# Optimization experiments

Hardware: AMD Instinct MI355X
Metric: run time of the kernel (lower is better)

The kernel has to match this reference:

```python
import jax, jax.numpy as jnp
import numpy as np
from jax import lax

K_ADA = 0.1
EPS = 1e-5
B, G = 2, 96
C0, C1, C2, C3, F = 1, 16, 32, 64, 64


def adanorm(x, g):
    # AdaNorm over the last (channel) axis: w * (1 - k*xn) * xn
    mean = x.mean(-1, keepdims=True)
    var = ((x - mean) ** 2).mean(-1, keepdims=True) + EPS
    xn = (x - mean) * lax.rsqrt(var)
    return g * (1.0 - K_ADA * xn) * xn


def conv3d(x, w, b, stride):
    # x: [B,D,H,W,Cin], w: [3,3,3,Cin,Cout], padding 1
    y = lax.conv_general_dilated(x, w, (stride,) * 3, [(1, 1)] * 3,
                                 dimension_numbers=('NDHWC', 'DHWIO', 'NDHWC'))
    return y + b


def downsample_mask(m):
    # active output sites of SparseConv3d(k=3, s=2, p=1): any active input in window
    return lax.reduce_window(m, 0.0, lax.max, (1, 3, 3, 3), (1, 2, 2, 2),
                             [(0, 0), (1, 1), (1, 1), (1, 1)])


def setup_inputs() -> dict:
    key = jax.random.key(0)
    ks = jax.random.split(key, 20)
    mask = (jax.random.uniform(ks[0], (B, G, G, G)) < 0.05).astype(jnp.float32)
    x = jax.random.normal(ks[1], (B, G, G, G, C0), jnp.float32) * mask[..., None]

    def wconv(k, cin, cout):
        return jax.random.normal(k, (3, 3, 3, cin, cout), jnp.float32) / np.sqrt(27.0 * cin)

    inp = {'x': x, 'mask': mask}
    chans = [(C0, C1), (C1, C2), (C2, C2), (C2, C3), (C3, C3)]
    for i, (ci, co) in enumerate(chans, start=1):
        inp[f'w{i}'] = wconv(ks[2 * i], ci, co)
        inp[f'b{i}'] = jax.random.normal(ks[2 * i + 1], (co,), jnp.float32) * 0.01
        inp[f'g{i}'] = jnp.ones((co,), jnp.float32)
    inp['wh'] = jax.random.normal(ks[12], (C3, F), jnp.float32) / np.sqrt(C3)
    inp['bh'] = jax.random.normal(ks[13], (F,), jnp.float32) * 0.01
    inp['gh'] = jnp.ones((F,), jnp.float32)
    return inp


def reference(x, mask, w1, b1, g1, w2, b2, g2, w3, b3, g3, w4, b4, g4, w5, b5, g5, wh, bh, gh):
    m1 = mask
    h = conv3d(x, w1, b1, 1) * m1[..., None]            # SubMConv3d
    h = jax.nn.relu(adanorm(h, g1)) * m1[..., None]
    m2 = downsample_mask(m1)
    h = conv3d(h, w2, b2, 2) * m2[..., None]            # SparseConv3d s=2
    h = jax.nn.relu(adanorm(h, g2)) * m2[..., None]
    h = conv3d(h, w3, b3, 1) * m2[..., None]            # SubMConv3d
    h = jax.nn.relu(adanorm(h, g3)) * m2[..., None]
    m3 = downsample_mask(m2)
    h = conv3d(h, w4, b4, 2) * m3[..., None]            # SparseConv3d s=2
    h = jax.nn.relu(adanorm(h, g4)) * m3[..., None]
    h = conv3d(h, w5, b5, 1) * m3[..., None]            # SubMConv3d
    h = jax.nn.relu(adanorm(h, g5)) * m3[..., None]
    # SparseGlobalMaxPool over active voxels
    neg = jnp.asarray(-3.0e38, h.dtype)
    pooled = jnp.where(m3[..., None] > 0, h, neg).max(axis=(1, 2, 3))  # [B, C3]
    # head: Linear -> AdaNorm -> ReLU -> Dropout(eval = identity)
    out = jax.nn.relu(adanorm(pooled @ wh + bh, gh))
    return out
```

## Files before the change

### kernel.cpp

```cpp
#include <hip/hip_runtime.h>
#include <math.h>

#define K_ADA 0.1f
#define NEPS 1e-5f

typedef __attribute__((ext_vector_type(8))) short short8;
typedef __attribute__((ext_vector_type(4))) float f32x4;
typedef unsigned short ushort_t;

__device__ __forceinline__ ushort_t f2b(float f) {
    union { float f; unsigned u; } v; v.f = f;
    unsigned r = (v.u + 0x7fffu + ((v.u >> 16) & 1u)) >> 16;
    return (ushort_t)r;
}

__device__ __forceinline__ float wave_sum64(float v) {
#pragma unroll
    for (int m = 1; m < 64; m <<= 1) v += __shfl_xor(v, m, 64);
    return v;
}

template <int CIN, int COUT>
__device__ __forceinline__ void pack_w_el(const float* __restrict__ w,
                                          ushort_t* __restrict__ wp, int t)
{
    constexpr int NKH = CIN / 32;
    constexpr int NCT = COUT / 16;
    int jj = t & 7;
    int lane = (t >> 3) & 63;
    int rest = t >> 9;
    int kh = rest % NKH;
    int rest2 = rest / NKH;
    int ct = rest2 % NCT;
    int tap = rest2 / NCT;
    int cin = kh * 32 + (lane >> 4) * 8 + jj;
    int cout = ct * 16 + (lane & 15);
    wp[t] = f2b(w[(tap * CIN + cin) * COUT + cout]);
}

__global__ __launch_bounds__(256) void prep_k(
    const float* __restrict__ w1, const float* __restrict__ w2,
    const float* __restrict__ w3, const float* __restrict__ w4,
    const float* __restrict__ w5, const float* __restrict__ m1,
    ushort_t* __restrict__ wp1, ushort_t* __restrict__ wp2,
    ushort_t* __restrict__ wp3, ushort_t* __restrict__ wp4,
    ushort_t* __restrict__ wp5, float* __restrict__ m2,
    float* __restrict__ zeropad)
{
    int t = blockIdx.x * 256 + threadIdx.x;
    if (t < 512) {
        int jj = t & 7;
        int lane = t >> 3;
        int tap = (lane >> 4) * 8 + jj;
        int cout = lane & 15;
        wp1[t] = (tap < 27) ? f2b(w1[tap * 16 + cout]) : (ushort_t)0;
    } else if (t < 14848) {
        int u = t - 512;
        int jj = u & 7;
        int lane = (u >> 3) & 63;
        int rest = u >> 9;
        int ct = rest & 1;
        int p = rest >> 1;
        int tap = 2 * p + (lane >> 5);
        int cin = ((lane >> 4) & 1) * 8 + jj;
        int cout = ct * 16 + (lane & 15);
        wp2[u] = (tap < 27) ? f2b(w2[(tap * 16 + cin) * 32 + cout]) : (ushort_t)0;
    } else if (t < 42496) {
        pack_w_el<32, 32>(w3, wp3, t - 14848);
    } else if (t < 97792) {
        pack_w_el<32, 64>(w4, wp4, t - 42496);
    } else if (t < 208384) {
        pack_w_el<64, 64>(w5, wp5, t - 97792);
    } else if (t < 429568) {
        int v = t - 208384;
        constexpr int GO = 48, GI = 96;
        int b = v / (GO * GO * GO);
        int r = v % (GO * GO * GO);
        int d = r / (GO * GO), h = (r / GO) % GO, x = r % GO;
        float mx = 0.f;
        for (int kd = 0; kd < 3; ++kd) {
            int zd = 2 * d + kd - 1; if ((unsigned)zd >= GI) continue;
            for (int kh = 0; kh < 3; ++kh) {
                int zh = 2 * h + kh - 1; if ((unsigned)zh >= GI) continue;
                for (int kw = 0; kw < 3; ++kw) {
                    int zx = 2 * x + kw - 1; if ((unsigned)zx >= GI) continue;
                    mx = fmaxf(mx, m1[((b * GI + zd) * GI + zh) * GI + zx]);
                }
            }
        }
        m2[v] = mx;
    } else if (t < 429576) {
        zeropad[t - 429568] = 0.f;
    }
}

template <int GO, int GI>
__global__ __launch_bounds__(256) void dmask_k(const float* __restrict__ mi,
                                               float* __restrict__ mo)
{
    constexpr int N = 2 * GO * GO * GO;
    int v = blockIdx.x * 256 + threadIdx.x;
    if (v >= N) return;
    int b = v / (GO * GO * GO);
    int r = v % (GO * GO * GO);
    int d = r / (GO * GO), h = (r / GO) % GO, x = r % GO;
    float mx = 0.f;
    for (int kd = 0; kd < 3; ++kd) {
        int zd = 2 * d + kd - 1; if ((unsigned)zd >= GI) continue;
        for (int kh = 0; kh < 3; ++kh) {
            int zh = 2 * h + kh - 1; if ((unsigned)zh >= GI) continue;
            for (int kw = 0; kw < 3; ++kw) {
                int zx = 2 * x + kw - 1; if ((unsigned)zx >= GI) continue;
                mx = fmaxf(mx, mi[((b * GI + zd) * GI + zh) * GI + zx]);
            }
        }
    }
    mo[v] = mx;
}

__global__ __launch_bounds__(256) void conv1_mfma_k(const float* __restrict__ x,
                                                    const float* __restrict__ m1,
                                                    const ushort_t* __restrict__ wp1,
                                                    const float* __restrict__ bias,
                                                    const float* __restrict__ gain,
                                                    const float* __restrict__ zerof,
                                                    ushort_t* __restrict__ h1b)
{
    constexpr int G = 96, G3 = G * G * G;
    int wave = (blockIdx.x * 256 + threadIdx.x) >> 6;
    int lane = threadIdx.x & 63;
    int m = lane & 15, q = lane >> 4;
    int vb = wave * 16;
    int vm = vb + m;
    int b = vm / G3;
    int rr = vm % G3;
    int dm = rr / (G * G), hm = (rr / G) % G, xm = rr % G;

    bool act = (m1[vm] != 0.f);
    if (!__any(act)) {
        reinterpret_cast<unsigned long long*>(h1b + (size_t)vb * 16)[lane] = 0ull;
        return;
    }

    float xs[8];
#pragma unroll
    for (int j = 0; j < 8; ++j) {
        int k = q * 8 + j;
        int kd = k / 9, kh = (k / 3) % 3, kw = k % 3;
        int id = dm + kd - 1, ih = hm + kh - 1, ix = xm + kw - 1;
        bool ok = (k < 27) && ((unsigned)id < (unsigned)G) &&
                  ((unsigned)ih < (unsigned)G) && ((unsigned)ix < (unsigned)G);
        const float* xp = ok ? (x + (((size_t)b * G + id) * G + ih) * G + ix) : zerof;
        xs[j] = *xp;
    }
    ushort_t av[8];
#pragma unroll
    for (int j = 0; j < 8; ++j) av[j] = f2b(xs[j]);
    short8 a = *reinterpret_cast<short8*>(av);
    short8 bfr = *reinterpret_cast<const short8*>(wp1 + lane * 8);
    f32x4 acc = {0.f, 0.f, 0.f, 0.f};
    acc = __builtin_amdgcn_mfma_f32_16x16x32_bf16(a, bfr, acc, 0, 0, 0);

    float bn = bias[m], gn = gain[m];
#pragma unroll
    for (int i = 0; i < 4; ++i) {
        int w = vb + q * 4 + i;
        float xv = acc[i] + bn;
        float s = xv;
#pragma unroll
        for (int mk = 1; mk < 16; mk <<= 1) s += __shfl_xor(s, mk, 64);
        float mean = s * (1.f / 16.f);
        float dd = xv - mean;
        float ss = dd * dd;
#pragma unroll
        for (int mk = 1; mk < 16; mk <<= 1) ss += __shfl_xor(ss, mk, 64);
        float rs = rsqrtf(ss * (1.f / 16.f) + NEPS);
        float xn = dd * rs;
        float o = fmaxf(gn * (1.f - K_ADA * xn) * xn, 0.f);
        h1b[(size_t)w * 16 + m] = (m1[w] != 0.f) ? f2b(o) : (ushort_t)0;
    }
}

__device__ __forceinline__ void norm32_epilogue(
    f32x4 acc0, f32x4 acc1, int vb, int q, int n,
    const float* __restrict__ bias, const float* __restrict__ gain,
    const float* __restrict__ mask, ushort_t* __restrict__ outb)
{
    float b0 = bias[n], b1 = bias[16 + n];
    float g0 = gain[n], g1 = gain[16 + n];
#pragma unroll
    for (int i = 0; i < 4; ++i) {
        int w = vb + q * 4 + i;
        float x0 = acc0[i] + b0;
        float x1 = acc1[i] + b1;
        float s = x0 + x1;
#pragma unroll
        for (int mk = 1; mk < 16; mk <<= 1) s += __shfl_xor(s, mk, 64);
        float mean = s * (1.f / 32.f);
        float d0 = x0 - mean, d1 = x1 - mean;
        float ss = d0 * d0 + d1 * d1;
#pragma unroll
        for (int mk = 1; mk < 16; mk <<= 1) ss += __shfl_xor(ss, mk, 64);
        float rs = rsqrtf(ss * (1.f / 32.f) + NEPS);
        float mv = mask[w];
        float xn0 = d0 * rs, xn1 = d1 * rs;
        float o0 = fmaxf(g0 * (1.f - K_ADA * xn0) * xn0, 0.f);
        float o1 = fmaxf(g1 * (1.f - K_ADA * xn1) * xn1, 0.f);
        if (mv == 0.f) { o0 = 0.f; o1 = 0.f; }
        outb[(size_t)w * 32 + n]      = f2b(o0);
        outb[(size_t)w * 32 + 16 + n] = f2b(o1);
    }
}

__global__ __launch_bounds__(256) void conv2_mfma_k(
    const ushort_t* __restrict__ h1b, const ushort_t* __restrict__ wp2,
    const float* __restrict__ bias, const float* __restrict__ gain,
    const float* __restrict__ m2, const ushort_t* __restrict__ zp,
    ushort_t* __restrict__ h2b)
{
    constexpr int G = 48, GI = 96, G3 = G * G * G;
    int wave = (blockIdx.x * 256 + threadIdx.x) >> 6;
    int lane = threadIdx.x & 63;
    int m = lane & 15, q = lane >> 4;
    int vb = wave * 32;
    int tq = q >> 1;
    int hq = q & 1;

    int vmA = vb + m, vmB = vb + 16 + m;
    int bA = vmA / G3, rA = vmA % G3;
    int dA = rA / (G * G), hA = (rA / G) % G, xA = rA % G;
    int bB = vmB / G3, rB = vmB % G3;
    int dB = rB / (G * G), hB = (rB / G) % G, xB = rB % G;

    f32x4 acc00 = {0.f, 0.f, 0.f, 0.f}, acc01 = acc00, acc10 = acc00, acc11 = acc00;
#pragma unroll
    for (int p = 0; p < 14; ++p) {
        int tap = 2 * p + tq;
        int kd = tap / 9, kh = (tap / 3) % 3, kw = tap % 3;
        int idA = 2 * dA + kd - 1, ihA = 2 * hA + kh - 1, ixA = 2 * xA + kw - 1;
        int idB = 2 * dB + kd - 1, ihB = 2 * hB + kh - 1, ixB = 2 * xB + kw - 1;
        bool okA = (tap < 27) && ((unsigned)idA < (unsigned)GI) &&
                   ((unsigned)ihA < (unsigned)GI) && ((unsigned)ixA < (unsigned)GI);
        bool okB = (tap < 27) && ((unsigned)idB < (unsigned)GI) &&
                   ((unsigned)ihB < (unsigned)GI) && ((unsigned)ixB < (unsigned)GI);
        size_t nvA = (((size_t)bA * GI + idA) * GI + ihA) * GI + ixA;
        size_t nvB = (((size_t)bB * GI + idB) * GI + ihB) * GI + ixB;
        const ushort_t* pA = okA ? (h1b + nvA * 16 + hq * 8) : zp;
        const ushort_t* pB = okB ? (h1b + nvB * 16 + hq * 8) : zp;
        short8 a0 = *reinterpret_cast<const short8*>(pA);
        short8 a1 = *reinterpret_cast<const short8*>(pB);
        short8 bv0 = *reinterpret_cast<const short8*>(wp2 + ((size_t)(p * 2 + 0) * 64 + lane) * 8);
        short8 bv1 = *reinterpret_cast<const short8*>(wp2 + ((size_t)(p * 2 + 1) * 64 + lane) * 8);
        acc00 = __builtin_amdgcn_mfma_f32_16x16x32_bf16(a0, bv0, acc00, 0, 0, 0);
        acc01 = __builtin_amdgcn_mfma_f32_16x16x32_bf16(a0, bv1, acc01, 0, 0, 0);
        acc10 = __builtin_amdgcn_mfma_f32_16x16x32_bf16(a1, bv0, acc10, 0, 0, 0);
        acc11 = __builtin_amdgcn_mfma_f32_16x16x32_bf16(a1, bv1, acc11, 0, 0, 0);
    }
    norm32_epilogue(acc00, acc01, vb,      q, m, bias, gain, m2, h2b);
    norm32_epilogue(acc10, acc11, vb + 16, q, m, bias, gain, m2, h2b);
}

__global__ __launch_bounds__(256, 4) void conv3_mfma_k(
    const ushort_t* __restrict__ h2b, const ushort_t* __restrict__ wp3,
    const float* __restrict__ bias, const float* __restrict__ gain,
    const float* __restrict__ m2, const ushort_t* __restrict__ zp,
    ushort_t* __restrict__ h3b)
{
    constexpr int G = 48, G3 = G * G * G;
    int wave = (blockIdx.x * 256 + threadIdx.x) >> 6;
    int lane = threadIdx.x & 63;
    int m = lane & 15, q = lane >> 4;
    int vb = wave * 32;

    int vmA = vb + m, vmB = vb + 16 + m;
    int bA = vmA / G3, rA = vmA % G3;
    int dA = rA / (G * G), hA = (rA / G) % G, xA = rA % G;
    int bB = vmB / G3, rB = vmB % G3;
    int dB = rB / (G * G), hB = (rB / G) % G, xB = rB % G;

    f32x4 acc00 = {0.f, 0.f, 0.f, 0.f}, acc01 = acc00, acc10 = acc00, acc11 = acc00;
#pragma unroll
    for (int tap = 0; tap < 27; ++tap) {
        const int kd = tap / 9, kh = (tap / 3) % 3, kw = tap % 3;
        int idA = dA + kd - 1, ihA = hA + kh - 1, ixA = xA + kw - 1;
        int idB = dB + kd - 1, ihB = hB + kh - 1, ixB = xB + kw - 1;
        bool okA = ((unsigned)idA < (unsigned)G) && ((unsigned)ihA < (unsigned)G) &&
                   ((unsigned)ixA < (unsigned)G);
        bool okB = ((unsigned)idB < (unsigned)G) && ((unsigned)ihB < (unsigned)G) &&
                   ((unsigned)ixB < (unsigned)G);
        size_t nvA = (((size_t)bA * G + idA) * G + ihA) * G + ixA;
        size_t nvB = (((size_t)bB * G + idB) * G + ihB) * G + ixB;
        const ushort_t* pA = okA ? (h2b + nvA * 32 + q * 8) : zp;
        const ushort_t* pB = okB ? (h2b + nvB * 32 + q * 8) : zp;
        short8 a0 = *reinterpret_cast<const short8*>(pA);
        short8 a1 = *reinterpret_cast<const short8*>(pB);
        short8 bv0 = *reinterpret_cast<const short8*>(wp3 + ((size_t)(tap * 2 + 0) * 64 + lane) * 8);
        short8 bv1 = *reinterpret_cast<const short8*>(wp3 + ((size_t)(tap * 2 + 1) * 64 + lane) * 8);
        acc00 = __builtin_amdgcn_mfma_f32_16x16x32_bf16(a0, bv0, acc00, 0, 0, 0);
        acc01 = __builtin_amdgcn_mfma_f32_16x16x32_bf16(a0, bv1, acc01, 0, 0, 0);
        acc10 = __builtin_amdgcn_mfma_f32_16x16x32_bf16(a1, bv0, acc10, 0, 0, 0);
        acc11 = __builtin_amdgcn_mfma_f32_16x16x32_bf16(a1, bv1, acc11, 0, 0, 0);
    }
    norm32_epilogue(acc00, acc01, vb,      q, m, bias, gain, m2, h3b);
    norm32_epilogue(acc10, acc11, vb + 16, q, m, bias, gain, m2, h3b);
}

template <int G_IN, int CIN, int STRIDE, bool OUTB>
__global__ __launch_bounds__(256, 4) void conv45_tile_k(
    const ushort_t* __restrict__ Ab, const ushort_t* __restrict__ Wp,
    const float* __restrict__ bias, const float* __restrict__ gain,
    const float* __restrict__ mask,
    ushort_t* __restrict__ outb, float* __restrict__ outf)
{
    constexpr int G = 24;
    constexpr int NKH = CIN / 32;
    constexpr int NCH = CIN / 8;
    constexpr int PADC = NCH + 1;
    constexpr int HD = STRIDE + 3;
    constexpr int HH = STRIDE + 3;
    constexpr int HX = 3 * STRIDE + 3;
    constexpr int NHV = HD * HH * HX;
    constexpr int NCHUNK = NHV * NCH;

    __shared__ __align__(16) ushort_t halo[NHV * PADC * 8];
    __shared__ float nbuf[16][65];

    int bid = blockIdx.x;
    int b = bid / 864;
    int r = bid % 864;
    int td = r / 72, th = (r / 6) % 12, tx = r % 6;
    int d0 = 2 * td, h0 = 2 * th, x0 = 4 * tx;
    int bd = d0 * STRIDE - 1, bh = h0 * STRIDE - 1, bx = x0 * STRIDE - 1;

    for (int c = threadIdx.x; c < NCHUNK; c += 256) {
        int hv = c / NCH, j = c % NCH;
        int gd = bd + hv / (HH * HX);
        int gh = bh + (hv / HX) % HH;
        int gx = bx + hv % HX;
        short8 val = {0, 0, 0, 0, 0, 0, 0, 0};
        if ((unsigned)gd < (unsigned)G_IN && (unsigned)gh < (unsigned)G_IN &&
            (unsigned)gx < (unsigned)G_IN)
            val = *reinterpret_cast<const short8*>(
                Ab + ((((size_t)b * G_IN + gd) * G_IN + gh) * G_IN + gx) * CIN + j * 8);
        *reinterpret_cast<short8*>(halo + ((size_t)hv * PADC + j) * 8) = val;
    }
    __syncthreads();

    int ct = threadIdx.x >> 6;
    int lane = threadIdx.x & 63;
    int m = lane & 15, q = lane >> 4;
    int md = (m >> 3) & 1, mh = (m >> 2) & 1, mx = m & 3;

    f32x4 acc = {0.f, 0.f, 0.f, 0.f};
    constexpr int NT = 27 * NKH;
    constexpr int GSZ = 9;
#pragma unroll
    for (int g = 0; g < NT / GSZ; ++g) {
        short8 ab[GSZ], bb[GSZ];
#pragma unroll
        for (int j = 0; j < GSZ; ++j) {
            int it = g * GSZ + j;
            int tap = it / NKH, k2 = it % NKH;
            const int kd = tap / 9, kh = (tap / 3) % 3, kw = tap % 3;
            int hv = ((md * STRIDE + kd) * HH + (mh * STRIDE + kh)) * HX +
                     (mx * STRIDE + kw);
            ab[j] = *reinterpret_cast<const short8*>(
                halo + ((size_t)hv * PADC + k2 * 4 + q) * 8);
            bb[j] = *reinterpret_cast<const short8*>(
                Wp + (((size_t)(tap * 4 + ct) * NKH + k2) * 64 + lane) * 8);
        }
#pragma unroll
        for (int j = 0; j < GSZ; ++j)
            acc = __builtin_amdgcn_mfma_f32_16x16x32_bf16(ab[j], bb[j], acc, 0, 0, 0);
    }

    float bn = bias[ct * 16 + m];
#pragma unroll
    for (int i = 0; i < 4; ++i) nbuf[q * 4 + i][ct * 16 + m] = acc[i] + bn;
    __syncthreads();

    float gn = gain[lane];
#pragma unroll
    for (int i = 0; i < 4; ++i) {
        int vloc = ct * 4 + i;
        int vd = d0 + ((vloc >> 3) & 1);
        int vh = h0 + ((vloc >> 2) & 1);
        int vx = x0 + (vloc & 3);
        int w = ((b * G + vd) * G + vh) * G + vx;
        float val = nbuf[vloc][lane];
        float mean = wave_sum64(val) * (1.f / 64.f);
        float dd = val - mean;
        float var = wave_sum64(dd * dd) * (1.f / 64.f) + NEPS;
        float xn = dd * rsqrtf(var);
        float o = fmaxf(gn * (1.f - K_ADA * xn) * xn, 0.f);
        if (mask[w] == 0.f) o = 0.f;
        if (OUTB) outb[(size_t)w * 64 + lane] = f2b(o);
        else      outf[(size_t)w * 64 + lane] = o;
    }
}

__global__ __launch_bounds__(256) void pool1_k(const float* __restrict__ h5,
                                               float* __restrict__ partials)
{
    int chunk = blockIdx.x % 54;
    int b = blockIdx.x / 54;
    int c = threadIdx.x & 63;
    int s = threadIdx.x >> 6;
    const float* base = h5 + ((size_t)b * 13824 + chunk * 256) * 64;
    float mx = 0.f;
#pragma unroll 4
    for (int v = s; v < 256; v += 4) mx = fmaxf(mx, base[v * 64 + c]);
    __shared__ float red[256];
    red[threadIdx.x] = mx;
    __syncthreads();
    if (s == 0)
        partials[blockIdx.x * 64 + c] =
            fmaxf(fmaxf(red[c], red[64 + c]), fmaxf(red[128 + c], red[192 + c]));
}

__global__ __launch_bounds__(128) void pool2_head_k(const float* __restrict__ partials,
                                                    const float* __restrict__ wh,
                                                    const float* __restrict__ bh,
                                                    const float* __restrict__ gh,
                                                    float* __restrict__ out)
{
    __shared__ float pooled[2][64];
    int t = threadIdx.x;
    int b = t >> 6;
    int f = t & 63;
    float mx = 0.f;
    for (int p = 0; p < 54; ++p) mx = fmaxf(mx, partials[(b * 54 + p) * 64 + f]);
    pooled[b][f] = mx;
    __syncthreads();
    float acc = bh[f];
#pragma unroll
    for (int k = 0; k < 64; ++k) acc += pooled[b][k] * wh[k * 64 + f];
    float mean = wave_sum64(acc) * (1.f / 64.f);
    float dd = acc - mean;
    float var = wave_sum64(dd * dd) * (1.f / 64.f) + NEPS;
    float xn = dd * rsqrtf(var);
    float val = gh[f] * (1.f - K_ADA * xn) * xn;
    out[t] = fmaxf(val, 0.f);
}

extern "C" void kernel_launch(void* const* d_in, const int* in_sizes, int n_in,
                              void* d_out, int out_size, void* d_ws, size_t ws_size,
                              hipStream_t stream)
{
    const float* x  = (const float*)d_in[0];
    const float* m1 = (const float*)d_in[1];
    const float* w1 = (const float*)d_in[2];
    const float* b1 = (const float*)d_in[3];
    const float* g1 = (const float*)d_in[4];
    const float* w2 = (const float*)d_in[5];
    const float* b2 = (const float*)d_in[6];
    const float* g2 = (const float*)d_in[7];
    const float* w3 = (const float*)d_in[8];
    const float* b3 = (const float*)d_in[9];
    const float* g3 = (const float*)d_in[10];
    const float* w4 = (const float*)d_in[11];
    const float* b4 = (const float*)d_in[12];
    const float* g4 = (const float*)d_in[13];
    const float* w5 = (const float*)d_in[14];
    const float* b5 = (const float*)d_in[15];
    const float* g5 = (const float*)d_in[16];
    const float* wh = (const float*)d_in[17];
    const float* bh = (const float*)d_in[18];
    const float* gh = (const float*)d_in[19];
    float* out = (float*)d_out;

    float* ws = (float*)d_ws;
    ushort_t* h1b = (ushort_t*)ws;
    ushort_t* h2b = (ushort_t*)(ws + 14155776);
    ushort_t* h3b = (ushort_t*)(ws + 17694720);
    ushort_t* h4b = (ushort_t*)(ws + 21233664);
    float* h5 = ws + 22118400;
    float* m2 = ws + 23887872;
    float* m3 = ws + 24109056;
    float* partials = ws + 24136704;
    ushort_t* wp1 = (ushort_t*)(ws + 24143616);
    ushort_t* wp2 = (ushort_t*)(ws + 24143872);
    ushort_t* wp3 = (ushort_t*)(ws + 24151040);
    ushort_t* wp4 = (ushort_t*)(ws + 24164864);
    ushort_t* wp5 = (ushort_t*)(ws + 24192512);
    float* zeropad = ws + 24247808;

    prep_k<<<1679, 256, 0, stream>>>(w1, w2, w3, w4, w5, m1,
                                     wp1, wp2, wp3, wp4, wp5, m2, zeropad);
    dmask_k<24, 48><<<108, 256, 0, stream>>>(m2, m3);

    const ushort_t* zp = (const ushort_t*)zeropad;
    conv1_mfma_k<<<27648, 256, 0, stream>>>(x, m1, wp1, b1, g1, zeropad, h1b);
    conv2_mfma_k<<<1728, 256, 0, stream>>>(h1b, wp2, b2, g2, m2, zp, h2b);
    conv3_mfma_k<<<1728, 256, 0, stream>>>(h2b, wp3, b3, g3, m2, zp, h3b);
    conv45_tile_k<48, 32, 2, true><<<1728, 256, 0, stream>>>(h3b, wp4, b4, g4, m3, h4b, nullptr);
    conv45_tile_k<24, 64, 1, false><<<1728, 256, 0, stream>>>(h4b, wp5, b5, g5, m3, nullptr, h5);

    pool1_k<<<108, 256, 0, stream>>>(h5, partials);
    pool2_head_k<<<1, 128, 0, stream>>>(partials, wh, bh, gh, out);
}
```

Before: 270.6 us.

## Compact active voxels for conv1 and stage LDS halo tiles for conv2/conv3

Conv1 is split into two kernels. A fill kernel zeros the output and builds a compacted list of active voxels using ballot and an atomic counter. A grid-stride kernel then runs the MFMA only on 16-voxel chunks of that list, skipping the partially inactive groups the old kernel still computed. Conv2 and conv3 are rewritten to load a 4x4x4 output tile's input halo into shared memory once and read all 27 taps from LDS, instead of issuing redundant global gathers per tap. This adds atomics, an extra launch and LDS pressure, and reuses the h2b workspace region to hold the list.

```diff
diff --git a/kernel.cpp b/kernel.cpp
--- a/kernel.cpp
+++ b/kernel.cpp
@@ -18,6 +18,10 @@
 #pragma unroll
     for (int m = 1; m < 64; m <<= 1) v += __shfl_xor(v, m, 64);
     return v;
+}
+
+__host__ __device__ constexpr int tapd2(int tap) {
+    return tap >= 27 ? 0 : (tap / 9) * 81 + ((tap / 3) % 3) * 9 + (tap % 3);
 }
 
 template <int CIN, int COUT>
@@ -45,7 +49,7 @@
     ushort_t* __restrict__ wp1, ushort_t* __restrict__ wp2,
     ushort_t* __restrict__ wp3, ushort_t* __restrict__ wp4,
     ushort_t* __restrict__ wp5, float* __restrict__ m2,
-    float* __restrict__ zeropad)
+    float* __restrict__ zeropad, int* __restrict__ counter)
 {
     int t = blockIdx.x * 256 + threadIdx.x;
     if (t < 512) {
@@ -91,6 +95,8 @@
         m2[v] = mx;
     } else if (t < 429576) {
         zeropad[t - 429568] = 0.f;
+    } else if (t == 429576) {
+        *counter = 0;
     }
 }
 
@@ -118,191 +124,264 @@
     mo[v] = mx;
 }
 
-__global__ __launch_bounds__(256) void conv1_mfma_k(const float* __restrict__ x,
-                                                    const float* __restrict__ m1,
-                                                    const ushort_t* __restrict__ wp1,
-                                                    const float* __restrict__ bias,
-                                                    const float* __restrict__ gain,
-                                                    const float* __restrict__ zerof,
-                                                    ushort_t* __restrict__ h1b)
+__global__ __launch_bounds__(256) void conv1_fill_k(const float* __restrict__ m1,
+                                                    ushort_t* __restrict__ h1b,
+                                                    int* __restrict__ list,
+                                                    int* __restrict__ counter)
+{
+    int v = blockIdx.x * 256 + threadIdx.x;
+    const short8 z = {0, 0, 0, 0, 0, 0, 0, 0};
+    short8* hp = reinterpret_cast<short8*>(h1b + (size_t)v * 16);
+    hp[0] = z; hp[1] = z;
+    bool act = (m1[v] != 0.f);
+    unsigned long long msk = __ballot(act);
+    int lane = threadIdx.x & 63;
+    int base = 0;
+    int cnt = __popcll(msk);
+    if (lane == 0 && cnt) base = atomicAdd(counter, cnt);
+    base = __shfl(base, 0, 64);
+    if (act) {
+        int pre = __popcll(msk & ((1ull << lane) - 1ull));
+        list[base + pre] = v;
+    }
+}
+
+__global__ __launch_bounds__(256) void conv1_act_k(const float* __restrict__ x,
+                                                   const int* __restrict__ list,
+                                                   const int* __restrict__ counter,
+                                                   const ushort_t* __restrict__ wp1,
+                                                   const float* __restrict__ bias,
+                                                   const float* __restrict__ gain,
+                                                   const float* __restrict__ zerof,
+                                                   ushort_t* __restrict__ h1b)
 {
     constexpr int G = 96, G3 = G * G * G;
-    int wave = (blockIdx.x * 256 + threadIdx.x) >> 6;
+    int nact = counter[0];
+    if (nact <= 0) return;
+    int gwave = (blockIdx.x * 256 + threadIdx.x) >> 6;
+    int nwaves = gridDim.x * 4;
     int lane = threadIdx.x & 63;
     int m = lane & 15, q = lane >> 4;
-    int vb = wave * 16;
-    int vm = vb + m;
-    int b = vm / G3;
-    int rr = vm % G3;
-    int dm = rr / (G * G), hm = (rr / G) % G, xm = rr % G;
-
-    bool act = (m1[vm] != 0.f);
-    if (!__any(act)) {
-        reinterpret_cast<unsigned long long*>(h1b + (size_t)vb * 16)[lane] = 0ull;
-        return;
-    }
-
-    float xs[8];
-#pragma unroll
-    for (int j = 0; j < 8; ++j) {
-        int k = q * 8 + j;
-        int kd = k / 9, kh = (k / 3) % 3, kw = k % 3;
-        int id = dm + kd - 1, ih = hm + kh - 1, ix = xm + kw - 1;
-        bool ok = (k < 27) && ((unsigned)id < (unsigned)G) &&
-                  ((unsigned)ih < (unsigned)G) && ((unsigned)ix < (unsigned)G);
-        const float* xp = ok ? (x + (((size_t)b * G + id) * G + ih) * G + ix) : zerof;
-        xs[j] = *xp;
-    }
-    ushort_t av[8];
-#pragma unroll
-    for (int j = 0; j < 8; ++j) av[j] = f2b(xs[j]);
-    short8 a = *reinterpret_cast<short8*>(av);
+    int nchunk = (nact + 15) >> 4;
+    float bn = bias[m], gn = gain[m];
     short8 bfr = *reinterpret_cast<const short8*>(wp1 + lane * 8);
-    f32x4 acc = {0.f, 0.f, 0.f, 0.f};
-    acc = __builtin_amdgcn_mfma_f32_16x16x32_bf16(a, bfr, acc, 0, 0, 0);
-
-    float bn = bias[m], gn = gain[m];
-#pragma unroll
-    for (int i = 0; i < 4; ++i) {
-        int w = vb + q * 4 + i;
-        float xv = acc[i] + bn;
-        float s = xv;
-#pragma unroll
-        for (int mk = 1; mk < 16; mk <<= 1) s += __shfl_xor(s, mk, 64);
-        float mean = s * (1.f / 16.f);
-        float dd = xv - mean;
-        float ss = dd * dd;
-#pragma unroll
-        for (int mk = 1; mk < 16; mk <<= 1) ss += __shfl_xor(ss, mk, 64);
-        float rs = rsqrtf(ss * (1.f / 16.f) + NEPS);
-        float xn = dd * rs;
-        float o = fmaxf(gn * (1.f - K_ADA * xn) * xn, 0.f);
-        h1b[(size_t)w * 16 + m] = (m1[w] != 0.f) ? f2b(o) : (ushort_t)0;
-    }
-}
-
-__device__ __forceinline__ void norm32_epilogue(
-    f32x4 acc0, f32x4 acc1, int vb, int q, int n,
-    const float* __restrict__ bias, const float* __restrict__ gain,
-    const float* __restrict__ mask, ushort_t* __restrict__ outb)
-{
-    float b0 = bias[n], b1 = bias[16 + n];
-    float g0 = gain[n], g1 = gain[16 + n];
-#pragma unroll
-    for (int i = 0; i < 4; ++i) {
-        int w = vb + q * 4 + i;
-        float x0 = acc0[i] + b0;
-        float x1 = acc1[i] + b1;
-        float s = x0 + x1;
-#pragma unroll
-        for (int mk = 1; mk < 16; mk <<= 1) s += __shfl_xor(s, mk, 64);
-        float mean = s * (1.f / 32.f);
-        float d0 = x0 - mean, d1 = x1 - mean;
-        float ss = d0 * d0 + d1 * d1;
-#pragma unroll
-        for (int mk = 1; mk < 16; mk <<= 1) ss += __shfl_xor(ss, mk, 64);
-        float rs = rsqrtf(ss * (1.f / 32.f) + NEPS);
-        float mv = mask[w];
-        float xn0 = d0 * rs, xn1 = d1 * rs;
-        float o0 = fmaxf(g0 * (1.f - K_ADA * xn0) * xn0, 0.f);
-        float o1 = fmaxf(g1 * (1.f - K_ADA * xn1) * xn1, 0.f);
-        if (mv == 0.f) { o0 = 0.f; o1 = 0.f; }
-        outb[(size_t)w * 32 + n]      = f2b(o0);
-        outb[(size_t)w * 32 + 16 + n] = f2b(o1);
-    }
-}
-
-__global__ __launch_bounds__(256) void conv2_mfma_k(
+
+    for (int chunk = gwave; chunk < nchunk; chunk += nwaves) {
+        int idx = chunk * 16 + m;
+        int vm = list[min(idx, nact - 1)];
+        int b = vm / G3;
+        int rr = vm % G3;
+        int dm = rr / (G * G), hm = (rr / G) % G, xm = rr % G;
+
+        float xs[8];
+#pragma unroll
+        for (int j = 0; j < 8; ++j) {
+            int k = q * 8 + j;
+            int kd = k / 9, kh = (k / 3) % 3, kw = k % 3;
+            int id = dm + kd - 1, ih = hm + kh - 1, ix = xm + kw - 1;
+            bool ok = (k < 27) && ((unsigned)id < (unsigned)G) &&
+                      ((unsigned)ih < (unsigned)G) && ((unsigned)ix < (unsigned)G);
+            const float* xp = ok ? (x + (((size_t)b * G + id) * G + ih) * G + ix) : zerof;
+            xs[j] = *xp;
+        }
+        ushort_t av[8];
+#pragma unroll
+        for (int j = 0; j < 8; ++j) av[j] = f2b(xs[j]);
+        short8 a = *reinterpret_cast<short8*>(av);
+        f32x4 acc = {0.f, 0.f, 0.f, 0.f};
+        acc = __builtin_amdgcn_mfma_f32_16x16x32_bf16(a, bfr, acc, 0, 0, 0);
+
+#pragma unroll
+        for (int i = 0; i < 4; ++i) {
+            int oidx = chunk * 16 + q * 4 + i;
+            float xv = acc[i] + bn;
+            float s = xv;
+#pragma unroll
+            for (int mk = 1; mk < 16; mk <<= 1) s += __shfl_xor(s, mk, 64);
+            float mean = s * (1.f / 16.f);
+            float dd = xv - mean;
+            float ss = dd * dd;
+#pragma unroll
+            for (int mk = 1; mk < 16; mk <<= 1) ss += __shfl_xor(ss, mk, 64);
+            float rs = rsqrtf(ss * (1.f / 16.f) + NEPS);
+            float xn = dd * rs;
+            float o = fmaxf(gn * (1.f - K_ADA * xn) * xn, 0.f);
+            if (oidx < nact) {
+                int w = list[oidx];
+                h1b[(size_t)w * 16 + m] = f2b(o);
+            }
+        }
+    }
+}
+
+__global__ __launch_bounds__(256, 4) void conv2_tile_k(
     const ushort_t* __restrict__ h1b, const ushort_t* __restrict__ wp2,
     const float* __restrict__ bias, const float* __restrict__ gain,
     const float* __restrict__ m2, const ushort_t* __restrict__ zp,
     ushort_t* __restrict__ h2b)
 {
-    constexpr int G = 48, GI = 96, G3 = G * G * G;
-    int wave = (blockIdx.x * 256 + threadIdx.x) >> 6;
+    constexpr int GI = 96, G = 48;
+    __shared__ __align__(16) ushort_t halo[729 * 3 * 8];
+
+    int bid = blockIdx.x;
+    int b = bid / 1728;
+    int r = bid % 1728;
+    int td = r / 144, th = (r / 12) % 12, tx = r % 12;
+    int d0 = 4 * td, h0 = 4 * th, x0 = 4 * tx;
+    int bd = 2 * d0 - 1, bh = 2 * h0 - 1, bx = 2 * x0 - 1;
+
+    for (int c = threadIdx.x; c < 1458; c += 256) {
+        int hv = c >> 1, j = c & 1;
+        int gd = bd + hv / 81;
+        int gh = bh + (hv / 9) % 9;
+        int gx = bx + hv % 9;
+        bool ok = ((unsigned)gd < (unsigned)GI) && ((unsigned)gh < (unsigned)GI) &&
+                  ((unsigned)gx < (unsigned)GI);
+        const ushort_t* p = ok ? (h1b + ((((size_t)b * GI + gd) * GI + gh) * GI + gx) * 16 + j * 8) : zp;
+        *reinterpret_cast<short8*>(halo + ((size_t)hv * 3 + j) * 8) =
+            *reinterpret_cast<const short8*>(p);
+    }
+    __syncthreads();
+
+    int wv = threadIdx.x >> 6;
     int lane = threadIdx.x & 63;
     int m = lane & 15, q = lane >> 4;
-    int vb = wave * 32;
-    int tq = q >> 1;
-    int hq = q & 1;
-
-    int vmA = vb + m, vmB = vb + 16 + m;
-    int bA = vmA / G3, rA = vmA % G3;
-    int dA = rA / (G * G), hA = (rA / G) % G, xA = rA % G;
-    int bB = vmB / G3, rB = vmB % G3;
-    int dB = rB / (G * G), hB = (rB / G) % G, xB = rB % G;
-
-    f32x4 acc00 = {0.f, 0.f, 0.f, 0.f}, acc01 = acc00, acc10 = acc00, acc11 = acc00;
-#pragma unroll
-    for (int p = 0; p < 14; ++p) {
-        int tap = 2 * p + tq;
-        int kd = tap / 9, kh = (tap / 3) % 3, kw = tap % 3;
-        int idA = 2 * dA + kd - 1, ihA = 2 * hA + kh - 1, ixA = 2 * xA + kw - 1;
-        int idB = 2 * dB + kd - 1, ihB = 2 * hB + kh - 1, ixB = 2 * xB + kw - 1;
-        bool okA = (tap < 27) && ((unsigned)idA < (unsigned)GI) &&
-                   ((unsigned)ihA < (unsigned)GI) && ((unsigned)ixA < (unsigned)GI);
-        bool okB = (tap < 27) && ((unsigned)idB < (unsigned)GI) &&
-                   ((unsigned)ihB < (unsigned)GI) && ((unsigned)ixB < (unsigned)GI);
-        size_t nvA = (((size_t)bA * GI + idA) * GI + ihA) * GI + ixA;
-        size_t nvB = (((size_t)bB * GI + idB) * GI + ihB) * GI + ixB;
-        const ushort_t* pA = okA ? (h1b + nvA * 16 + hq * 8) : zp;
-        const ushort_t* pB = okB ? (h1b + nvB * 16 + hq * 8) : zp;
-        short8 a0 = *reinterpret_cast<const short8*>(pA);
-        short8 a1 = *reinterpret_cast<const short8*>(pB);
-        short8 bv0 = *reinterpret_cast<const short8*>(wp2 + ((size_t)(p * 2 + 0) * 64 + lane) * 8);
-        short8 bv1 = *reinterpret_cast<const short8*>(wp2 + ((size_t)(p * 2 + 1) * 64 + lane) * 8);
-        acc00 = __builtin_amdgcn_mfma_f32_16x16x32_bf16(a0, bv0, acc00, 0, 0, 0);
-        acc01 = __builtin_amdgcn_mfma_f32_16x16x32_bf16(a0, bv1, acc01, 0, 0, 0);
-        acc10 = __builtin_amdgcn_mfma_f32_16x16x32_bf16(a1, bv0, acc10, 0, 0, 0);
-        acc11 = __builtin_amdgcn_mfma_f32_16x16x32_bf16(a1, bv1, acc11, 0, 0, 0);
-    }
-    norm32_epilogue(acc00, acc01, vb,      q, m, bias, gain, m2, h2b);
-    norm32_epilogue(acc10, acc11, vb + 16, q, m, bias, gain, m2, h2b);
-}
-
-__global__ __launch_bounds__(256, 4) void conv3_mfma_k(
+    int mh = m >> 2, mx = m & 3;
+    int tq = q >> 1, hq = q & 1;
+    int hbase = 162 * wv + 18 * mh + 2 * mx;
+
+    f32x4 accs[2];
+#pragma unroll
+    for (int ct = 0; ct < 2; ++ct) {
+        f32x4 acc = {0.f, 0.f, 0.f, 0.f};
+#pragma unroll
+        for (int g = 0; g < 2; ++g) {
+            short8 ab[7], bb[7];
+#pragma unroll
+            for (int j = 0; j < 7; ++j) {
+                const int p = g * 7 + j;
+                int hv = hbase + (tq ? tapd2(2 * p + 1) : tapd2(2 * p));
+                ab[j] = *reinterpret_cast<const short8*>(halo + ((size_t)hv * 3 + hq) * 8);
+                bb[j] = *reinterpret_cast<const short8*>(
+                    wp2 + ((size_t)(p * 2 + ct) * 64 + lane) * 8);
+            }
+#pragma unroll
+            for (int j = 0; j < 7; ++j)
+                acc = __builtin_amdgcn_mfma_f32_16x16x32_bf16(ab[j], bb[j], acc, 0, 0, 0);
+        }
+        accs[ct] = acc;
+    }
+
+    float b0 = bias[m], b1 = bias[16 + m];
+    float g0 = gain[m], g1 = gain[16 + m];
+#pragma unroll
+    for (int i = 0; i < 4; ++i) {
+        int rr2 = q * 4 + i;
+        int w = ((b * G + d0 + wv) * G + h0 + (rr2 >> 2)) * G + x0 + (rr2 & 3);
+        float xv0 = accs[0][i] + b0;
+        float xv1 = accs[1][i] + b1;
+        float s = xv0 + xv1;
+#pragma unroll
+        for (int mk = 1; mk < 16; mk <<= 1) s += __shfl_xor(s, mk, 64);
+        float mean = s * (1.f / 32.f);
+        float dd0 = xv0 - mean, dd1 = xv1 - mean;
+        float ss = dd0 * dd0 + dd1 * dd1;
+#pragma unroll
+        for (int mk = 1; mk < 16; mk <<= 1) ss += __shfl_xor(ss, mk, 64);
+        float rs = rsqrtf(ss * (1.f / 32.f) + NEPS);
+        float mv = m2[w];
+        float xn0 = dd0 * rs, xn1 = dd1 * rs;
+        float o0 = fmaxf(g0 * (1.f - K_ADA * xn0) * xn0, 0.f);
+        float o1 = fmaxf(g1 * (1.f - K_ADA * xn1) * xn1, 0.f);
+        if (mv == 0.f) { o0 = 0.f; o1 = 0.f; }
+        h2b[(size_t)w * 32 + m]      = f2b(o0);
+        h2b[(size_t)w * 32 + 16 + m] = f2b(o1);
+    }
+}
+
+__global__ __launch_bounds__(256, 4) void conv3_tile_k(
     const ushort_t* __restrict__ h2b, const ushort_t* __restrict__ wp3,
     const float* __restrict__ bias, const float* __restrict__ gain,
     const float* __restrict__ m2, const ushort_t* __restrict__ zp,
     ushort_t* __restrict__ h3b)
 {
-    constexpr int G = 48, G3 = G * G * G;
-    int wave = (blockIdx.x * 256 + threadIdx.x) >> 6;
+    constexpr int G = 48;
+    __shared__ __align__(16) ushort_t halo[216 * 5 * 8];
+
+    int bid = blockIdx.x;
+    int b = bid / 1728;
+    int r = bid % 1728;
+    int td = r / 144, th = (r / 12) % 12, tx = r % 12;
+    int d0 = 4 * td, h0 = 4 * th, x0 = 4 * tx;
+    int bd = d0 - 1, bh = h0 - 1, bx = x0 - 1;
+
+    for (int c = threadIdx.x; c < 864; c += 256) {
+        int hv = c >> 2, j = c & 3;
+        int gd = bd + hv / 36;
+        int gh = bh + (hv / 6) % 6;
+        int gx = bx + hv % 6;
+        bool ok = ((unsigned)gd < (unsigned)G) && ((unsigned)gh < (unsigned)G) &&
+                  ((unsigned)gx < (unsigned)G);
+        const ushort_t* p = ok ? (h2b + ((((size_t)b * G + gd) * G + gh) * G + gx) * 32 + j * 8) : zp;
+        *reinterpret_cast<short8*>(halo + ((size_t)hv * 5 + j) * 8) =
+            *reinterpret_cast<const short8*>(p);
+    }
+    __syncthreads();
+
+    int wv = threadIdx.x >> 6;
     int lane = threadIdx.x & 63;
     int m = lane & 15, q = lane >> 4;
-    int vb = wave * 32;
-
-    int vmA = vb + m, vmB = vb + 16 + m;
-    int bA = vmA / G3, rA = vmA % G3;
-    int dA = rA / (G * G), hA = (rA / G) % G, xA = rA % G;
-    int bB = vmB / G3, rB = vmB % G3;
-    int dB = rB / (G * G), hB = (rB / G) % G, xB = rB % G;
-
-    f32x4 acc00 = {0.f, 0.f, 0.f, 0.f}, acc01 = acc00, acc10 = acc00, acc11 = acc00;
-#pragma unroll
-    for (int tap = 0; tap < 27; ++tap) {
-        const int kd = tap / 9, kh = (tap / 3) % 3, kw = tap % 3;
-        int idA = dA + kd - 1, ihA = hA + kh - 1, ixA = xA + kw - 1;
-        int idB = dB + kd - 1, ihB = hB + kh - 1, ixB = xB + kw - 1;
-        bool okA = ((unsigned)idA < (unsigned)G) && ((unsigned)ihA < (unsigned)G) &&
-                   ((unsigned)ixA < (unsigned)G);
-        bool okB = ((unsigned)idB < (unsigned)G) && ((unsigned)ihB < (unsigned)G) &&
-                   ((unsigned)ixB < (unsigned)G);
-        size_t nvA = (((size_t)bA * G + idA) * G + ihA) * G + ixA;
-        size_t nvB = (((size_t)bB * G + idB) * G + ihB) * G + ixB;
-        const ushort_t* pA = okA ? (h2b + nvA * 32 + q * 8) : zp;
-        const ushort_t* pB = okB ? (h2b + nvB * 32 + q * 8) : zp;
-        short8 a0 = *reinterpret_cast<const short8*>(pA);
-        short8 a1 = *reinterpret_cast<const short8*>(pB);
-        short8 bv0 = *reinterpret_cast<const short8*>(wp3 + ((size_t)(tap * 2 + 0) * 64 + lane) * 8);
-        short8 bv1 = *reinterpret_cast<const short8*>(wp3 + ((size_t)(tap * 2 + 1) * 64 + lane) * 8);
-        acc00 = __builtin_amdgcn_mfma_f32_16x16x32_bf16(a0, bv0, acc00, 0, 0, 0);
-        acc01 = __builtin_amdgcn_mfma_f32_16x16x32_bf16(a0, bv1, acc01, 0, 0, 0);
-        acc10 = __builtin_amdgcn_mfma_f32_16x16x32_bf16(a1, bv0, acc10, 0, 0, 0);
-        acc11 = __builtin_amdgcn_mfma_f32_16x16x32_bf16(a1, bv1, acc11, 0, 0, 0);
-    }
-    norm32_epilogue(acc00, acc01, vb,      q, m, bias, gain, m2, h3b);
-    norm32_epilogue(acc10, acc11, vb + 16, q, m, bias, gain, m2, h3b);
+    int mh = m >> 2, mx = m & 3;
+    int hbase = 36 * wv + 6 * mh + mx;
+
+    f32x4 accs[2];
+#pragma unroll
+    for (int ct = 0; ct < 2; ++ct) {
+        f32x4 acc = {0.f, 0.f, 0.f, 0.f};
+#pragma unroll
+        for (int g = 0; g < 3; ++g) {
+            short8 ab[9], bb[9];
+#pragma unroll
+            for (int j = 0; j < 9; ++j) {
+                const int tap = g * 9 + j;
+                const int kd = tap / 9, kh = (tap / 3) % 3, kw = tap % 3;
+                int hv = hbase + kd * 36 + kh * 6 + kw;
+                ab[j] = *reinterpret_cast<const short8*>(halo + ((size_t)hv * 5 + q) * 8);
+                bb[j] = *reinterpret_cast<const short8*>(
+                    wp3 + ((size_t)(tap * 2 + ct) * 64 + lane) * 8);
+            }
+#pragma unroll
+            for (int j = 0; j < 9; ++j)
+                acc = __builtin_amdgcn_mfma_f32_16x16x32_bf16(ab[j], bb[j], acc, 0, 0, 0);
+        }
+        accs[ct] = acc;
+    }
+
+    float b0 = bias[m], b1 = bias[16 + m];
+    float g0 = gain[m], g1 = gain[16 + m];
+#pragma unroll
+    for (int i = 0; i < 4; ++i) {
+        int rr2 = q * 4 + i;
+        int w = ((b * G + d0 + wv) * G + h0 + (rr2 >> 2)) * G + x0 + (rr2 & 3);
+        float xv0 = accs[0][i] + b0;
+        float xv1 = accs[1][i] + b1;
+        float s = xv0 + xv1;
+#pragma unroll
+        for (int mk = 1; mk < 16; mk <<= 1) s += __shfl_xor(s, mk, 64);
+        float mean = s * (1.f / 32.f);
+        float dd0 = xv0 - mean, dd1 = xv1 - mean;
+        float ss = dd0 * dd0 + dd1 * dd1;
+#pragma unroll
+        for (int mk = 1; mk < 16; mk <<= 1) ss += __shfl_xor(ss, mk, 64);
+        float rs = rsqrtf(ss * (1.f / 32.f) + NEPS);
+        float mv = m2[w];
+        float xn0 = dd0 * rs, xn1 = dd1 * rs;
+        float o0 = fmaxf(g0 * (1.f - K_ADA * xn0) * xn0, 0.f);
+        float o1 = fmaxf(g1 * (1.f - K_ADA * xn1) * xn1, 0.f);
+        if (mv == 0.f) { o0 = 0.f; o1 = 0.f; }
+        h3b[(size_t)w * 32 + m]      = f2b(o0);
+        h3b[(size_t)w * 32 + 16 + m] = f2b(o1);
+    }
 }
 
 template <int G_IN, int CIN, int STRIDE, bool OUTB>
@@ -484,15 +563,18 @@
     ushort_t* wp4 = (ushort_t*)(ws + 24164864);
     ushort_t* wp5 = (ushort_t*)(ws + 24192512);
     float* zeropad = ws + 24247808;
+    int* counter = (int*)(ws + 24247816);
+    int* list = (int*)(ws + 14155776);
 
     prep_k<<<1679, 256, 0, stream>>>(w1, w2, w3, w4, w5, m1,
-                                     wp1, wp2, wp3, wp4, wp5, m2, zeropad);
+                                     wp1, wp2, wp3, wp4, wp5, m2, zeropad, counter);
     dmask_k<24, 48><<<108, 256, 0, stream>>>(m2, m3);
 
     const ushort_t* zp = (const ushort_t*)zeropad;
-    conv1_mfma_k<<<27648, 256, 0, stream>>>(x, m1, wp1, b1, g1, zeropad, h1b);
-    conv2_mfma_k<<<1728, 256, 0, stream>>>(h1b, wp2, b2, g2, m2, zp, h2b);
-    conv3_mfma_k<<<1728, 256, 0, stream>>>(h2b, wp3, b3, g3, m2, zp, h3b);
+    conv1_fill_k<<<6912, 256, 0, stream>>>(m1, h1b, list, counter);
+    conv1_act_k<<<864, 256, 0, stream>>>(x, list, counter, wp1, b1, g1, zeropad, h1b);
+    conv2_tile_k<<<3456, 256, 0, stream>>>(h1b, wp2, b2, g2, m2, zp, h2b);
+    conv3_tile_k<<<3456, 256, 0, stream>>>(h2b, wp3, b3, g3, m2, zp, h3b);
     conv45_tile_k<48, 32, 2, true><<<1728, 256, 0, stream>>>(h3b, wp4, b4, g4, m3, h4b, nullptr);
     conv45_tile_k<24, 64, 1, false><<<1728, 256, 0, stream>>>(h4b, wp5, b5, g5, m3, nullptr, h5);
 
```

Result: slower. 541.4 us (+100.1%).
